# Kernel tuning notes

Hardware: AMD Instinct MI355X
Metric: run time of the kernel (lower is better)

Reference implementation:

```python
import jax, jax.numpy as jnp
import numpy as np

N = 100_000          # num nodes
E = 1_600_000        # undirected edges (mean_degree = 2E/N = 32)
Q = 8                # num_groups
NUM_ITER = 5         # fixed BP iterations (max_num_iter)


def setup_inputs() -> dict:
    key = jax.random.key(0)
    k1, k2, k3, k4 = jax.random.split(key, 4)
    u = jax.random.randint(k1, (E,), 0, N, dtype=jnp.int32)
    v = jax.random.randint(k2, (E,), 0, N, dtype=jnp.int32)
    # directed messages: both orientations of every undirected edge
    src = jnp.concatenate([u, v])                 # [2E] message source i of i->j
    dst = jnp.concatenate([v, u])                 # [2E] message target j of i->j
    # rev[e] = index of the reverse message j->i for edge e = i->j
    rev = jnp.concatenate([jnp.arange(E, 2 * E, dtype=jnp.int32),
                           jnp.arange(E, dtype=jnp.int32)])
    psi0 = jax.random.uniform(k3, (N, Q), dtype=jnp.float32)
    msg0 = jax.random.uniform(k4, (2 * E, Q), dtype=jnp.float32)
    c = 2.0 * E / N  # mean degree
    beta = jnp.asarray(np.log(Q / np.sqrt(c - 1.0) + 1.0), dtype=jnp.float32)
    return dict(beta=beta, psi0=psi0, msg0=msg0, src=src, dst=dst, rev=rev,
                num_iter=NUM_ITER)


def reference(beta, psi0, msg0, src, dst, rev, num_iter):
    N_, Q_ = psi0.shape
    M = msg0.shape[0]
    mean_w = M / (N_ * N_)  # adjacency_matrix.mean() = 2E / N^2 (unweighted)
    psi = psi0 / psi0.sum(1, keepdims=True)   # normalized marginals [N,Q]
    msg = msg0 / msg0.sum(1, keepdims=True)   # normalized messages  [M,Q]
    h = (-beta * mean_w * psi).sum(0)         # external field        [Q]

    def step(carry, _):
        msg, psi, h = carry
        c = jnp.expm1(beta)                          # e^beta - 1
        # per-incoming-edge factor, in log space (scatter_mul -> segment_sum of logs)
        log_f = jnp.log1p(msg * c)                   # [M,Q]
        S = jax.ops.segment_sum(log_f, dst, num_segments=N_)  # [N,Q] prod over k->i
        # message i->j: exclude contribution of reverse edge j->i (cavity)
        logits = h + S[src] - log_f[rev]             # [M,Q]
        new_msg = jax.nn.softmax(logits, axis=-1)    # normalized per message
        diff = jnp.max(jnp.abs(new_msg - msg))
        # marginals from updated messages
        log_f2 = jnp.log1p(new_msg * c)
        S2 = jax.ops.segment_sum(log_f2, dst, num_segments=N_)
        new_psi = jax.nn.softmax(h + S2, axis=-1)    # [N,Q]
        new_h = (-beta * mean_w * new_psi).sum(0)    # [Q]
        return (new_msg, new_psi, new_h), diff

    (msg, psi, h), diffs = jax.lax.scan(step, (msg, psi, h), None, length=int(num_iter))
    return msg, psi, diffs[-1]
```

## Files before the change

### kernel.cpp

```cpp
#include <hip/hip_runtime.h>
#include <math.h>

#define Q 8
#define NUM_ITER 5
#define BLOCK 256
#define EBLK 1024
#define BLOCKA 512
#define NBN 1024
#define NBSHIFT 10
#define MAXBKT 128
#define W 4
#define QS 262144.0f
#define GRED 512

__device__ __forceinline__ void load8(const float* __restrict__ p, float v[Q]) {
    float4 a = ((const float4*)p)[0];
    float4 b = ((const float4*)p)[1];
    v[0]=a.x; v[1]=a.y; v[2]=a.z; v[3]=a.w;
    v[4]=b.x; v[5]=b.y; v[6]=b.z; v[7]=b.w;
}

__device__ __forceinline__ void store8(float* __restrict__ p, const float v[Q]) {
    ((float4*)p)[0] = make_float4(v[0],v[1],v[2],v[3]);
    ((float4*)p)[1] = make_float4(v[4],v[5],v[6],v[7]);
}

__device__ __forceinline__ void softmax8_fast(float l[Q]) {
    float mx = l[0];
    #pragma unroll
    for (int q=1;q<Q;q++) mx = fmaxf(mx, l[q]);
    float s = 0.f;
    #pragma unroll
    for (int q=0;q<Q;q++) { l[q] = __expf(l[q]-mx); s += l[q]; }
    float inv = 1.0f/s;
    #pragma unroll
    for (int q=0;q<Q;q++) l[q] *= inv;
}

__device__ __forceinline__ void pack18(const float lf[Q], int loc, uint4& a, unsigned& x) {
    unsigned v[Q];
    #pragma unroll
    for (int q=0;q<Q;q++) v[q] = (unsigned)__float2int_rn(lf[q]*QS);
    a.x = (v[0]&0xFFFFu) | ((v[1]&0xFFFFu)<<16);
    a.y = (v[2]&0xFFFFu) | ((v[3]&0xFFFFu)<<16);
    a.z = (v[4]&0xFFFFu) | ((v[5]&0xFFFFu)<<16);
    a.w = (v[6]&0xFFFFu) | ((v[7]&0xFFFFu)<<16);
    x = (v[0]>>16) | ((v[1]>>16)<<2) | ((v[2]>>16)<<4) | ((v[3]>>16)<<6)
      | ((v[4]>>16)<<8) | ((v[5]>>16)<<10) | ((v[6]>>16)<<12) | ((v[7]>>16)<<14)
      | ((unsigned)loc<<16);
}

__device__ __forceinline__ void dq18(uint4 a, unsigned x, float lf[Q]) {
    lf[0] = (float)((a.x & 0xFFFFu) | ((x     &3u)<<16)) * (1.0f/QS);
    lf[1] = (float)((a.x >> 16)     | (((x>>2 )&3u)<<16)) * (1.0f/QS);
    lf[2] = (float)((a.y & 0xFFFFu) | (((x>>4 )&3u)<<16)) * (1.0f/QS);
    lf[3] = (float)((a.y >> 16)     | (((x>>6 )&3u)<<16)) * (1.0f/QS);
    lf[4] = (float)((a.z & 0xFFFFu) | (((x>>8 )&3u)<<16)) * (1.0f/QS);
    lf[5] = (float)((a.z >> 16)     | (((x>>10)&3u)<<16)) * (1.0f/QS);
    lf[6] = (float)((a.w & 0xFFFFu) | (((x>>12)&3u)<<16)) * (1.0f/QS);
    lf[7] = (float)((a.w >> 16)     | (((x>>14)&3u)<<16)) * (1.0f/QS);
}

__global__ __launch_bounds__(EBLK) void k_cnt2(const int* __restrict__ src,
                                               const int* __restrict__ dst,
                                               int* __restrict__ gcnt, int E) {
    __shared__ int cnt[MAXBKT];
    int tid = threadIdx.x;
    for (int t=tid; t<MAXBKT; t+=EBLK) cnt[t]=0;
    __syncthreads();
    int k = blockIdx.x*EBLK + tid;
    if (k < E) {
        atomicAdd(&cnt[dst[k]>>NBSHIFT], 1);
        atomicAdd(&cnt[src[k]>>NBSHIFT], 1);
    }
    __syncthreads();
    for (int t=tid; t<MAXBKT; t+=EBLK) gcnt[(size_t)blockIdx.x*MAXBKT + t] = cnt[t];
}

__global__ __launch_bounds__(256) void k_scan2(const int* __restrict__ gcnt,
                                               int* __restrict__ erel,
                                               int* __restrict__ btot, int nblk) {
    int b = blockIdx.x;
    int t = threadIdx.x;
    int chunk = (nblk + 255) / 256;
    int lo = t*chunk, hi = lo+chunk; if (hi > nblk) hi = nblk; if (lo > nblk) lo = nblk;
    int s = 0;
    for (int i=lo;i<hi;++i) s += gcnt[(size_t)i*MAXBKT + b];
    __shared__ int part[256];
    part[t] = s;
    __syncthreads();
    for (int off=1; off<256; off<<=1) {
        int v = (t>=off) ? part[t-off] : 0;
        __syncthreads();
        part[t] += v;
        __syncthreads();
    }
    int base = (t==0) ? 0 : part[t-1];
    for (int i=lo;i<hi;++i) {
        int c = gcnt[(size_t)i*MAXBKT + b];
        erel[(size_t)i*MAXBKT + b] = base;
        base += c;
    }
    if (t==255) btot[b] = part[255];
}

__global__ void k_scan(const int* __restrict__ btot, int* __restrict__ bucket_start,
                       int nbkt) {
    if (threadIdx.x==0 && blockIdx.x==0) {
        int run = 0;
        for (int b=0;b<nbkt;b++) { bucket_start[b]=run; run += btot[b]; }
        bucket_start[nbkt] = run;
    }
}

__global__ void k_psi_init(const float* __restrict__ psi0,
                           const float* __restrict__ beta_p,
                           float mean_w, double* __restrict__ h0, int N) {
    int i = blockIdx.x*BLOCK + threadIdx.x;
    float c[Q];
    #pragma unroll
    for (int q=0;q<Q;q++) c[q]=0.f;
    if (i < N) {
        float p[Q]; load8(psi0 + (size_t)i*Q, p);
        float s = 0.f;
        #pragma unroll
        for (int q=0;q<Q;q++) s += p[q];
        float scale = -beta_p[0]*mean_w/s;
        #pragma unroll
        for (int q=0;q<Q;q++) c[q] = p[q]*scale;
    }
    __shared__ double sm[BLOCK/64][Q];
    #pragma unroll
    for (int q=0;q<Q;q++) {
        double x = (double)c[q];
        #pragma unroll
        for (int off=32;off;off>>=1) x += __shfl_down(x,off);
        if ((threadIdx.x&63)==0) sm[threadIdx.x>>6][q]=x;
    }
    __syncthreads();
    if (threadIdx.x < Q) {
        double x = sm[0][threadIdx.x]+sm[1][threadIdx.x]+sm[2][threadIdx.x]+sm[3][threadIdx.x];
        atomicAdd(h0+threadIdx.x, x);
    }
}

__global__ __launch_bounds__(EBLK) void k_init(const float* __restrict__ msg0,
                       const int* __restrict__ src, const int* __restrict__ dst,
                       const float* __restrict__ beta_p,
                       uint4* __restrict__ lfe_q, unsigned* __restrict__ lfe_x,
                       uint4* __restrict__ ebuf_q, unsigned* __restrict__ ebuf_x,
                       const int* __restrict__ erel,
                       const int* __restrict__ bucket_start_g, int E) {
    __shared__ int cnt[MAXBKT], excl[MAXBKT], base[MAXBKT];
    __shared__ int totsh;
    __shared__ uint4 staged[2*EBLK];
    __shared__ unsigned staged_x[2*EBLK];
    __shared__ int gpos[2*EBLK];
    int tid = threadIdx.x;
    for (int t=tid; t<MAXBKT; t+=EBLK) cnt[t]=0;
    if (tid < MAXBKT) base[tid] = bucket_start_g[tid] + erel[(size_t)blockIdx.x*MAXBKT + tid];
    __syncthreads();
    int k = blockIdx.x*EBLK + tid;
    bool act = (k < E);
    int b1=0,b2=0,o1=0,o2=0;
    uint4 p1, p2; unsigned x1, x2;
    if (act) {
        float cc = expm1f(beta_p[0]);
        int i = src[k], j = dst[k];
        float a[Q], b[Q];
        load8(msg0 + (size_t)k*Q, a);
        load8(msg0 + ((size_t)k+E)*Q, b);
        float sa=0.f, sb=0.f;
        #pragma unroll
        for (int q=0;q<Q;q++) { sa += a[q]; sb += b[q]; }
        float ia = 1.0f/sa, ib = 1.0f/sb;
        #pragma unroll
        for (int q=0;q<Q;q++) { a[q]*=ia; b[q]*=ib; }
        float lfa[Q], lfb[Q];
        #pragma unroll
        for (int q=0;q<Q;q++) {
            lfa[q] = __logf(fmaf(a[q], cc, 1.0f));
            lfb[q] = __logf(fmaf(b[q], cc, 1.0f));
        }
        b1 = j>>NBSHIFT; b2 = i>>NBSHIFT;
        o1 = atomicAdd(&cnt[b1], 1);
        o2 = atomicAdd(&cnt[b2], 1);
        pack18(lfa, j & (NBN-1), p1, x1);
        pack18(lfb, i & (NBN-1), p2, x2);
        lfe_q[k]   = p1; lfe_x[k]   = x1;
        lfe_q[k+E] = p2; lfe_x[k+E] = x2;
    }
    __syncthreads();
    if (tid < 64) {
        int a = cnt[2*tid], b = cnt[2*tid+1];
        int s = a+b;
        int incl = s;
        #pragma unroll
        for (int d=1; d<64; d<<=1) {
            int v = __shfl_up(incl, d);
            if (tid >= d) incl += v;
        }
        int exclp = incl - s;
        excl[2*tid]   = exclp;
        excl[2*tid+1] = exclp + a;
        if (tid==63) totsh = incl;
    }
    __syncthreads();
    if (act) {
        int s1 = excl[b1]+o1; staged[s1]=p1; staged_x[s1]=x1; gpos[s1]=base[b1]+o1;
        int s2 = excl[b2]+o2; staged[s2]=p2; staged_x[s2]=x2; gpos[s2]=base[b2]+o2;
    }
    __syncthreads();
    int total = totsh;
    for (int s=tid; s<total; s+=EBLK) {
        int g = gpos[s];
        ebuf_q[g] = staged[s];
        ebuf_x[g] = staged_x[s];
    }
}

template<bool LAST>
__global__ __launch_bounds__(EBLK) void k_edge(const int* __restrict__ src,
                       const int* __restrict__ dst,
                       const float* __restrict__ beta_p,
                       const double* __restrict__ h, const float* __restrict__ Sf,
                       uint4* __restrict__ lfe_q, unsigned* __restrict__ lfe_x,
                       float* __restrict__ out_msg,
                       uint4* __restrict__ ebuf_q, unsigned* __restrict__ ebuf_x,
                       const int* __restrict__ erel,
                       const int* __restrict__ bucket_start_g,
                       float* __restrict__ diff_out, int E) {
    __shared__ int cnt[MAXBKT], excl[MAXBKT], base[MAXBKT];
    __shared__ int totsh;
    __shared__ uint4 staged[2*EBLK];
    __shared__ unsigned staged_x[2*EBLK];
    __shared__ int gpos[2*EBLK];
    int tid = threadIdx.x;
    for (int t=tid; t<MAXBKT; t+=EBLK) cnt[t]=0;
    if (tid < MAXBKT) base[tid] = bucket_start_g[tid] + erel[(size_t)blockIdx.x*MAXBKT + tid];
    __syncthreads();
    int k = blockIdx.x*EBLK + tid;
    bool act = (k < E);
    float lmax = 0.f;
    int b1=0,b2=0,o1=0,o2=0;
    uint4 p1, p2; unsigned x1, x2;
    if (act) {
        float cc = expm1f(beta_p[0]);
        int i = src[k], j = dst[k];
        float lf1o[Q], lf2o[Q];
        dq18(lfe_q[k],   lfe_x[k],   lf1o);
        dq18(lfe_q[k+E], lfe_x[k+E], lf2o);
        float hv[Q];
        #pragma unroll
        for (int q=0;q<Q;q++) hv[q] = (float)h[q];
        float Si[Q], Sj[Q];
        load8(Sf + (size_t)i*Q, Si);
        load8(Sf + (size_t)j*Q, Sj);
        float l1[Q], l2[Q];
        #pragma unroll
        for (int q=0;q<Q;q++) {
            l1[q] = hv[q] + Si[q] - lf2o[q];
            l2[q] = hv[q] + Sj[q] - lf1o[q];
        }
        softmax8_fast(l1);
        softmax8_fast(l2);
        if (LAST) {
            float icc = 1.0f/cc;
            #pragma unroll
            for (int q=0;q<Q;q++) {
                float m1o = (__expf(lf1o[q]) - 1.0f) * icc;
                float m2o = (__expf(lf2o[q]) - 1.0f) * icc;
                lmax = fmaxf(lmax, fabsf(l1[q]-m1o));
                lmax = fmaxf(lmax, fabsf(l2[q]-m2o));
            }
            store8(out_msg + (size_t)k*Q,     l1);
            store8(out_msg + ((size_t)k+E)*Q, l2);
        }
        float lf1n[Q], lf2n[Q];
        #pragma unroll
        for (int q=0;q<Q;q++) {
            lf1n[q] = __logf(fmaf(l1[q], cc, 1.0f));
            lf2n[q] = __logf(fmaf(l2[q], cc, 1.0f));
        }
        b1 = j>>NBSHIFT; b2 = i>>NBSHIFT;
        o1 = atomicAdd(&cnt[b1], 1);
        o2 = atomicAdd(&cnt[b2], 1);
        pack18(lf1n, j & (NBN-1), p1, x1);
        pack18(lf2n, i & (NBN-1), p2, x2);
        lfe_q[k]   = p1; lfe_x[k]   = x1;
        lfe_q[k+E] = p2; lfe_x[k+E] = x2;
    }
    __syncthreads();
    if (tid < 64) {
        int a = cnt[2*tid], b = cnt[2*tid+1];
        int s = a+b;
        int incl = s;
        #pragma unroll
        for (int d=1; d<64; d<<=1) {
            int v = __shfl_up(incl, d);
            if (tid >= d) incl += v;
        }
        int exclp = incl - s;
        excl[2*tid]   = exclp;
        excl[2*tid+1] = exclp + a;
        if (tid==63) totsh = incl;
    }
    __syncthreads();
    if (act) {
        int s1 = excl[b1]+o1; staged[s1]=p1; staged_x[s1]=x1; gpos[s1]=base[b1]+o1;
        int s2 = excl[b2]+o2; staged[s2]=p2; staged_x[s2]=x2; gpos[s2]=base[b2]+o2;
    }
    __syncthreads();
    int total = totsh;
    for (int s=tid; s<total; s+=EBLK) {
        int g = gpos[s];
        ebuf_q[g] = staged[s];
        ebuf_x[g] = staged_x[s];
    }
    if (LAST) {
        float x = lmax;
        #pragma unroll
        for (int off=32;off;off>>=1) x = fmaxf(x, __shfl_down(x,off));
        __shared__ float smx[EBLK/64];
        if ((tid&63)==0) smx[tid>>6]=x;
        __syncthreads();
        if (tid==0) {
            float bmax = smx[0];
            #pragma unroll
            for (int t=1;t<EBLK/64;t++) bmax = fmaxf(bmax, smx[t]);
            atomicMax((unsigned int*)diff_out, __float_as_uint(bmax));
        }
    }
}

__global__ __launch_bounds__(BLOCKA) void k_accum(const uint4* __restrict__ ebuf_q,
                                                  const unsigned* __restrict__ ebuf_x,
                                                  const int* __restrict__ bucket_start,
                                                  unsigned long long* __restrict__ partials) {
    __shared__ unsigned long long Sl[NBN*4];
    int wg = blockIdx.x;
    int b = wg / W, w = wg % W;
    for (int t=threadIdx.x*4; t<NBN*8; t+=BLOCKA*4) *(int4*)((int*)Sl+t) = make_int4(0,0,0,0);
    __syncthreads();
    int lo = bucket_start[b], hi = bucket_start[b+1];
    int len = hi - lo;
    int l0 = lo + (int)(((long long)len * w) / W);
    int l1 = lo + (int)(((long long)len * (w+1)) / W);
    for (int s = l0 + threadIdx.x; s < l1; s += BLOCKA) {
        uint4 v = ebuf_q[s];
        unsigned x = ebuf_x[s];
        int loc = (int)(x >> 16);
        unsigned long long v0 = (v.x&0xFFFFu) | ((x&3u)<<16);
        unsigned long long v1 = (v.x>>16)     | (((x>>2)&3u)<<16);
        unsigned long long v2 = (v.y&0xFFFFu) | (((x>>4)&3u)<<16);
        unsigned long long v3 = (v.y>>16)     | (((x>>6)&3u)<<16);
        unsigned long long v4 = (v.z&0xFFFFu) | (((x>>8)&3u)<<16);
        unsigned long long v5 = (v.z>>16)     | (((x>>10)&3u)<<16);
        unsigned long long v6 = (v.w&0xFFFFu) | (((x>>12)&3u)<<16);
        unsigned long long v7 = (v.w>>16)     | (((x>>14)&3u)<<16);
        unsigned long long* p = Sl + loc*4;
        atomicAdd(p+0, v0 | (v1<<32));
        atomicAdd(p+1, v2 | (v3<<32));
        atomicAdd(p+2, v4 | (v5<<32));
        atomicAdd(p+3, v6 | (v7<<32));
    }
    __syncthreads();
    unsigned long long* outp = partials + (size_t)wg * (NBN*4);
    for (int t=threadIdx.x*4; t<NBN*8; t+=BLOCKA*4) *(int4*)((int*)outp+t) = *(const int4*)((const int*)Sl+t);
}

template<bool INIT, bool LAST>
__global__ __launch_bounds__(BLOCK) void k_reduce(const unsigned* __restrict__ pu,
                         const double* __restrict__ hcur,
                         const float* __restrict__ beta_p,
                         float mean_w, double* __restrict__ hnext,
                         float* __restrict__ Sf, float* __restrict__ psi_out, int N) {
    int q = threadIdx.x & 7;
    float hq = 0.f;
    if (!INIT) hq = (float)hcur[q];
    double pacc = 0.0;
    int total = N*8;
    int stride = BLOCK*GRED;
    for (int gid = blockIdx.x*BLOCK + threadIdx.x; gid < total; gid += stride) {
        int i = gid >> 3;
        int b = i >> NBSHIFT, loc = i & (NBN-1);
        unsigned s = 0;
        #pragma unroll
        for (int w=0; w<W; ++w) s += pu[(size_t)(b*W+w)*(NBN*8) + loc*8 + q];
        float Sv = (float)s * (1.0f/QS);
        Sf[gid] = Sv;
        if (!INIT) {
            float l = hq + Sv;
            float mx = l;
            #pragma unroll
            for (int m8=1;m8<8;m8<<=1) mx = fmaxf(mx, __shfl_xor(mx, m8));
            float ex = __expf(l - mx);
            float sum = ex;
            #pragma unroll
            for (int m8=1;m8<8;m8<<=1) sum += __shfl_xor(sum, m8);
            float p = ex / sum;
            if (LAST) psi_out[gid] = p;
            pacc += (double)p;
        }
    }
    if (!INIT) {
        double x = pacc;
        #pragma unroll
        for (int m8=8;m8<64;m8<<=1) x += __shfl_xor(x, m8);
        __shared__ double sm[BLOCK/64][Q];
        if ((threadIdx.x&63) < Q) sm[threadIdx.x>>6][threadIdx.x&7] = x;
        __syncthreads();
        if (threadIdx.x < Q) {
            double t = sm[0][threadIdx.x]+sm[1][threadIdx.x]+sm[2][threadIdx.x]+sm[3][threadIdx.x];
            double scale = -(double)beta_p[0]*(double)mean_w;
            atomicAdd(hnext+threadIdx.x, t*scale);
        }
    }
}

extern "C" void kernel_launch(void* const* d_in, const int* in_sizes, int n_in,
                              void* d_out, int out_size, void* d_ws, size_t ws_size,
                              hipStream_t stream) {
    const float* beta = (const float*)d_in[0];
    const float* psi0 = (const float*)d_in[1];
    const float* msg0 = (const float*)d_in[2];
    const int*   src  = (const int*)d_in[3];
    const int*   dst  = (const int*)d_in[4];

    int N = in_sizes[1] / Q;
    int M = in_sizes[2] / Q;
    int E = M / 2;
    int nbkt = (N + NBN - 1) / NBN;
    float mean_w = (float)((double)M / ((double)N * (double)N));

    float* out_msg  = (float*)d_out;
    float* out_psi  = out_msg + (size_t)M*Q;
    float* out_diff = out_psi + (size_t)N*Q;

    int geE = (E + EBLK-1)/EBLK;

    char* p = (char*)d_ws;
    double* hb[2];
    hb[0] = (double*)p;                      p += 2*Q*sizeof(double);
    hb[1] = hb[0] + Q;
    unsigned long long* partials = (unsigned long long*)p;  p += (size_t)nbkt*W*NBN*4*sizeof(unsigned long long);
    float* Sf = (float*)p;                   p += (size_t)N*Q*sizeof(float);
    uint4* lfe_q = (uint4*)p;                p += (size_t)M*sizeof(uint4);
    uint4* ebuf_q = (uint4*)p;               p += (size_t)M*sizeof(uint4);
    unsigned* lfe_x = (unsigned*)p;          p += (size_t)M*sizeof(unsigned);
    unsigned* ebuf_x = (unsigned*)p;         p += (size_t)M*sizeof(unsigned);
    int* gcnt = (int*)p;                     p += (size_t)geE*MAXBKT*sizeof(int);
    int* erel = (int*)p;                     p += (size_t)geE*MAXBKT*sizeof(int);
    int* btot = (int*)p;                     p += MAXBKT*sizeof(int);
    int* bucket_start = (int*)p;             p += (MAXBKT+1)*sizeof(int);

    int gn   = (N + BLOCK-1)/BLOCK;
    int gacc = nbkt * W;

    hipMemsetAsync(hb[0], 0, Q*sizeof(double), stream);

    k_cnt2<<<geE,EBLK,0,stream>>>(src, dst, gcnt, E);
    k_scan2<<<nbkt,256,0,stream>>>(gcnt, erel, btot, geE);
    k_scan<<<1,64,0,stream>>>(btot, bucket_start, nbkt);

    k_init<<<geE,EBLK,0,stream>>>(msg0, src, dst, beta, lfe_q, lfe_x, ebuf_q, ebuf_x,
                                  erel, bucket_start, E);
    k_psi_init<<<gn,BLOCK,0,stream>>>(psi0, beta, mean_w, hb[0], N);
    k_accum<<<gacc,BLOCKA,0,stream>>>(ebuf_q, ebuf_x, bucket_start, partials);
    k_reduce<true,false><<<GRED,BLOCK,0,stream>>>((const unsigned*)partials, hb[0], beta,
                                                  mean_w, hb[1], Sf, out_psi, N);

    int cur = 0;
    for (int t=0; t<NUM_ITER; ++t) {
        int nxt = cur^1;
        hipMemsetAsync(hb[nxt], 0, Q*sizeof(double), stream);
        if (t == NUM_ITER-1) {
            hipMemsetAsync(out_diff, 0, sizeof(float), stream);
            k_edge<true ><<<geE,EBLK,0,stream>>>(src,dst,beta,hb[cur],Sf,lfe_q,lfe_x,out_msg,
                                                 ebuf_q,ebuf_x,erel,bucket_start,out_diff,E);
            k_accum<<<gacc,BLOCKA,0,stream>>>(ebuf_q, ebuf_x, bucket_start, partials);
            k_reduce<false,true ><<<GRED,BLOCK,0,stream>>>((const unsigned*)partials, hb[cur], beta,
                                                           mean_w, hb[nxt], Sf, out_psi, N);
        } else {
            k_edge<false><<<geE,EBLK,0,stream>>>(src,dst,beta,hb[cur],Sf,lfe_q,lfe_x,out_msg,
                                                 ebuf_q,ebuf_x,erel,bucket_start,out_diff,E);
            k_accum<<<gacc,BLOCKA,0,stream>>>(ebuf_q, ebuf_x, bucket_start, partials);
            k_reduce<false,false><<<GRED,BLOCK,0,stream>>>((const unsigned*)partials, hb[cur], beta,
                                                           mean_w, hb[nxt], Sf, out_psi, N);
        }
        cur = nxt;
    }
}
```

Baseline: 579.3 us.

## Cache bucketed scatter positions once in init and reuse them in edge kernels

The init kernel now computes each edge's destination slot in the bucketed edge buffer with shared atomics, writes straight to global memory, and records both slots in a new per-edge position array. The iterative edge kernel loads these cached positions and scatters directly. This drops the per-iteration shared-memory counting, block scan, staging and three barriers. In exchange the scatter writes are no longer grouped by bucket within the block, so they are less coalesced, and each edge reads an extra 8 bytes per iteration.

```diff
diff --git a/kernel.cpp b/kernel.cpp
--- a/kernel.cpp
+++ b/kernel.cpp
@@ -149,22 +149,18 @@
                        const float* __restrict__ beta_p,
                        uint4* __restrict__ lfe_q, unsigned* __restrict__ lfe_x,
                        uint4* __restrict__ ebuf_q, unsigned* __restrict__ ebuf_x,
+                       int2* __restrict__ epos,
                        const int* __restrict__ erel,
                        const int* __restrict__ bucket_start_g, int E) {
-    __shared__ int cnt[MAXBKT], excl[MAXBKT], base[MAXBKT];
-    __shared__ int totsh;
-    __shared__ uint4 staged[2*EBLK];
-    __shared__ unsigned staged_x[2*EBLK];
-    __shared__ int gpos[2*EBLK];
+    __shared__ int cnt[MAXBKT], base[MAXBKT];
     int tid = threadIdx.x;
-    for (int t=tid; t<MAXBKT; t+=EBLK) cnt[t]=0;
-    if (tid < MAXBKT) base[tid] = bucket_start_g[tid] + erel[(size_t)blockIdx.x*MAXBKT + tid];
+    if (tid < MAXBKT) {
+        cnt[tid] = 0;
+        base[tid] = bucket_start_g[tid] + erel[(size_t)blockIdx.x*MAXBKT + tid];
+    }
     __syncthreads();
     int k = blockIdx.x*EBLK + tid;
-    bool act = (k < E);
-    int b1=0,b2=0,o1=0,o2=0;
-    uint4 p1, p2; unsigned x1, x2;
-    if (act) {
+    if (k < E) {
         float cc = expm1f(beta_p[0]);
         int i = src[k], j = dst[k];
         float a[Q], b[Q];
@@ -182,40 +178,17 @@
             lfa[q] = __logf(fmaf(a[q], cc, 1.0f));
             lfb[q] = __logf(fmaf(b[q], cc, 1.0f));
         }
-        b1 = j>>NBSHIFT; b2 = i>>NBSHIFT;
-        o1 = atomicAdd(&cnt[b1], 1);
-        o2 = atomicAdd(&cnt[b2], 1);
+        uint4 p1, p2; unsigned x1, x2;
         pack18(lfa, j & (NBN-1), p1, x1);
         pack18(lfb, i & (NBN-1), p2, x2);
         lfe_q[k]   = p1; lfe_x[k]   = x1;
         lfe_q[k+E] = p2; lfe_x[k+E] = x2;
-    }
-    __syncthreads();
-    if (tid < 64) {
-        int a = cnt[2*tid], b = cnt[2*tid+1];
-        int s = a+b;
-        int incl = s;
-        #pragma unroll
-        for (int d=1; d<64; d<<=1) {
-            int v = __shfl_up(incl, d);
-            if (tid >= d) incl += v;
-        }
-        int exclp = incl - s;
-        excl[2*tid]   = exclp;
-        excl[2*tid+1] = exclp + a;
-        if (tid==63) totsh = incl;
-    }
-    __syncthreads();
-    if (act) {
-        int s1 = excl[b1]+o1; staged[s1]=p1; staged_x[s1]=x1; gpos[s1]=base[b1]+o1;
-        int s2 = excl[b2]+o2; staged[s2]=p2; staged_x[s2]=x2; gpos[s2]=base[b2]+o2;
-    }
-    __syncthreads();
-    int total = totsh;
-    for (int s=tid; s<total; s+=EBLK) {
-        int g = gpos[s];
-        ebuf_q[g] = staged[s];
-        ebuf_x[g] = staged_x[s];
+        int b1 = j>>NBSHIFT, b2 = i>>NBSHIFT;
+        int g1 = base[b1] + atomicAdd(&cnt[b1], 1);
+        int g2 = base[b2] + atomicAdd(&cnt[b2], 1);
+        ebuf_q[g1] = p1; ebuf_x[g1] = x1;
+        ebuf_q[g2] = p2; ebuf_x[g2] = x2;
+        epos[k] = make_int2(g1, g2);
     }
 }
 
@@ -227,24 +200,12 @@
                        uint4* __restrict__ lfe_q, unsigned* __restrict__ lfe_x,
                        float* __restrict__ out_msg,
                        uint4* __restrict__ ebuf_q, unsigned* __restrict__ ebuf_x,
-                       const int* __restrict__ erel,
-                       const int* __restrict__ bucket_start_g,
+                       const int2* __restrict__ epos,
                        float* __restrict__ diff_out, int E) {
-    __shared__ int cnt[MAXBKT], excl[MAXBKT], base[MAXBKT];
-    __shared__ int totsh;
-    __shared__ uint4 staged[2*EBLK];
-    __shared__ unsigned staged_x[2*EBLK];
-    __shared__ int gpos[2*EBLK];
     int tid = threadIdx.x;
-    for (int t=tid; t<MAXBKT; t+=EBLK) cnt[t]=0;
-    if (tid < MAXBKT) base[tid] = bucket_start_g[tid] + erel[(size_t)blockIdx.x*MAXBKT + tid];
-    __syncthreads();
     int k = blockIdx.x*EBLK + tid;
-    bool act = (k < E);
     float lmax = 0.f;
-    int b1=0,b2=0,o1=0,o2=0;
-    uint4 p1, p2; unsigned x1, x2;
-    if (act) {
+    if (k < E) {
         float cc = expm1f(beta_p[0]);
         int i = src[k], j = dst[k];
         float lf1o[Q], lf2o[Q];
@@ -282,40 +243,14 @@
             lf1n[q] = __logf(fmaf(l1[q], cc, 1.0f));
             lf2n[q] = __logf(fmaf(l2[q], cc, 1.0f));
         }
-        b1 = j>>NBSHIFT; b2 = i>>NBSHIFT;
-        o1 = atomicAdd(&cnt[b1], 1);
-        o2 = atomicAdd(&cnt[b2], 1);
+        uint4 p1, p2; unsigned x1, x2;
         pack18(lf1n, j & (NBN-1), p1, x1);
         pack18(lf2n, i & (NBN-1), p2, x2);
         lfe_q[k]   = p1; lfe_x[k]   = x1;
         lfe_q[k+E] = p2; lfe_x[k+E] = x2;
-    }
-    __syncthreads();
-    if (tid < 64) {
-        int a = cnt[2*tid], b = cnt[2*tid+1];
-        int s = a+b;
-        int incl = s;
-        #pragma unroll
-        for (int d=1; d<64; d<<=1) {
-            int v = __shfl_up(incl, d);
-            if (tid >= d) incl += v;
-        }
-        int exclp = incl - s;
-        excl[2*tid]   = exclp;
-        excl[2*tid+1] = exclp + a;
-        if (tid==63) totsh = incl;
-    }
-    __syncthreads();
-    if (act) {
-        int s1 = excl[b1]+o1; staged[s1]=p1; staged_x[s1]=x1; gpos[s1]=base[b1]+o1;
-        int s2 = excl[b2]+o2; staged[s2]=p2; staged_x[s2]=x2; gpos[s2]=base[b2]+o2;
-    }
-    __syncthreads();
-    int total = totsh;
-    for (int s=tid; s<total; s+=EBLK) {
-        int g = gpos[s];
-        ebuf_q[g] = staged[s];
-        ebuf_x[g] = staged_x[s];
+        int2 gp = epos[k];
+        ebuf_q[gp.x] = p1; ebuf_x[gp.x] = x1;
+        ebuf_q[gp.y] = p2; ebuf_x[gp.y] = x2;
     }
     if (LAST) {
         float x = lmax;
@@ -449,6 +384,7 @@
     uint4* ebuf_q = (uint4*)p;               p += (size_t)M*sizeof(uint4);
     unsigned* lfe_x = (unsigned*)p;          p += (size_t)M*sizeof(unsigned);
     unsigned* ebuf_x = (unsigned*)p;         p += (size_t)M*sizeof(unsigned);
+    int2* epos = (int2*)p;                   p += (size_t)E*sizeof(int2);
     int* gcnt = (int*)p;                     p += (size_t)geE*MAXBKT*sizeof(int);
     int* erel = (int*)p;                     p += (size_t)geE*MAXBKT*sizeof(int);
     int* btot = (int*)p;                     p += MAXBKT*sizeof(int);
@@ -464,7 +400,7 @@
     k_scan<<<1,64,0,stream>>>(btot, bucket_start, nbkt);
 
     k_init<<<geE,EBLK,0,stream>>>(msg0, src, dst, beta, lfe_q, lfe_x, ebuf_q, ebuf_x,
-                                  erel, bucket_start, E);
+                                  epos, erel, bucket_start, E);
     k_psi_init<<<gn,BLOCK,0,stream>>>(psi0, beta, mean_w, hb[0], N);
     k_accum<<<gacc,BLOCKA,0,stream>>>(ebuf_q, ebuf_x, bucket_start, partials);
     k_reduce<true,false><<<GRED,BLOCK,0,stream>>>((const unsigned*)partials, hb[0], beta,
@@ -477,13 +413,13 @@
         if (t == NUM_ITER-1) {
             hipMemsetAsync(out_diff, 0, sizeof(float), stream);
             k_edge<true ><<<geE,EBLK,0,stream>>>(src,dst,beta,hb[cur],Sf,lfe_q,lfe_x,out_msg,
-                                                 ebuf_q,ebuf_x,erel,bucket_start,out_diff,E);
+                                                 ebuf_q,ebuf_x,epos,out_diff,E);
             k_accum<<<gacc,BLOCKA,0,stream>>>(ebuf_q, ebuf_x, bucket_start, partials);
             k_reduce<false,true ><<<GRED,BLOCK,0,stream>>>((const unsigned*)partials, hb[cur], beta,
                                                            mean_w, hb[nxt], Sf, out_psi, N);
         } else {
             k_edge<false><<<geE,EBLK,0,stream>>>(src,dst,beta,hb[cur],Sf,lfe_q,lfe_x,out_msg,
-                                                 ebuf_q,ebuf_x,erel,bucket_start,out_diff,E);
+                                                 ebuf_q,ebuf_x,epos,out_diff,E);
             k_accum<<<gacc,BLOCKA,0,stream>>>(ebuf_q, ebuf_x, bucket_start, partials);
             k_reduce<false,false><<<GRED,BLOCK,0,stream>>>((const unsigned*)partials, hb[cur], beta,
                                                            mean_w, hb[nxt], Sf, out_psi, N);
```

Result: slower. 700.4 us (+20.9%).

## Map one directed message per thread in edge kernel, exchanging reverse via lane shuffle

Applied to the files above, without the earlier changes.

The edge kernel now gives each thread one directed message instead of both orientations of an undirected edge. Lanes 0-31 handle the forward direction and lanes 32-63 the reverse direction of the same pair, and the reverse log-factor and node are exchanged with a cross-half-wave shuffle. The per-block pair count drops to 512 so that the bucket counts from the preprocessing kernels still match the edge kernel's block partition. This doubles thread count and lowers per-thread register and shared-memory use to raise occupancy and parallelism, at the cost of more blocks and finer-grained scatter staging.

```diff
diff --git a/kernel.cpp b/kernel.cpp
--- a/kernel.cpp
+++ b/kernel.cpp
@@ -4,7 +4,8 @@
 #define Q 8
 #define NUM_ITER 5
 #define BLOCK 256
-#define EBLK 1024
+#define PBLK 512
+#define EBLKT 1024
 #define BLOCKA 512
 #define NBN 1024
 #define NBSHIFT 10
@@ -61,20 +62,20 @@
     lf[7] = (float)((a.w >> 16)     | (((x>>14)&3u)<<16)) * (1.0f/QS);
 }
 
-__global__ __launch_bounds__(EBLK) void k_cnt2(const int* __restrict__ src,
+__global__ __launch_bounds__(PBLK) void k_cnt2(const int* __restrict__ src,
                                                const int* __restrict__ dst,
                                                int* __restrict__ gcnt, int E) {
     __shared__ int cnt[MAXBKT];
     int tid = threadIdx.x;
-    for (int t=tid; t<MAXBKT; t+=EBLK) cnt[t]=0;
-    __syncthreads();
-    int k = blockIdx.x*EBLK + tid;
-    if (k < E) {
-        atomicAdd(&cnt[dst[k]>>NBSHIFT], 1);
-        atomicAdd(&cnt[src[k]>>NBSHIFT], 1);
-    }
-    __syncthreads();
-    for (int t=tid; t<MAXBKT; t+=EBLK) gcnt[(size_t)blockIdx.x*MAXBKT + t] = cnt[t];
+    if (tid < MAXBKT) cnt[tid]=0;
+    __syncthreads();
+    int p = blockIdx.x*PBLK + tid;
+    if (p < E) {
+        atomicAdd(&cnt[dst[p]>>NBSHIFT], 1);
+        atomicAdd(&cnt[src[p]>>NBSHIFT], 1);
+    }
+    __syncthreads();
+    if (tid < MAXBKT) gcnt[(size_t)blockIdx.x*MAXBKT + tid] = cnt[tid];
 }
 
 __global__ __launch_bounds__(256) void k_scan2(const int* __restrict__ gcnt,
@@ -144,7 +145,7 @@
     }
 }
 
-__global__ __launch_bounds__(EBLK) void k_init(const float* __restrict__ msg0,
+__global__ __launch_bounds__(PBLK) void k_init(const float* __restrict__ msg0,
                        const int* __restrict__ src, const int* __restrict__ dst,
                        const float* __restrict__ beta_p,
                        uint4* __restrict__ lfe_q, unsigned* __restrict__ lfe_x,
@@ -153,23 +154,25 @@
                        const int* __restrict__ bucket_start_g, int E) {
     __shared__ int cnt[MAXBKT], excl[MAXBKT], base[MAXBKT];
     __shared__ int totsh;
-    __shared__ uint4 staged[2*EBLK];
-    __shared__ unsigned staged_x[2*EBLK];
-    __shared__ int gpos[2*EBLK];
+    __shared__ uint4 staged[2*PBLK];
+    __shared__ unsigned staged_x[2*PBLK];
+    __shared__ int gpos[2*PBLK];
     int tid = threadIdx.x;
-    for (int t=tid; t<MAXBKT; t+=EBLK) cnt[t]=0;
-    if (tid < MAXBKT) base[tid] = bucket_start_g[tid] + erel[(size_t)blockIdx.x*MAXBKT + tid];
-    __syncthreads();
-    int k = blockIdx.x*EBLK + tid;
-    bool act = (k < E);
+    if (tid < MAXBKT) {
+        cnt[tid] = 0;
+        base[tid] = bucket_start_g[tid] + erel[(size_t)blockIdx.x*MAXBKT + tid];
+    }
+    __syncthreads();
+    int p = blockIdx.x*PBLK + tid;
+    bool act = (p < E);
     int b1=0,b2=0,o1=0,o2=0;
     uint4 p1, p2; unsigned x1, x2;
     if (act) {
         float cc = expm1f(beta_p[0]);
-        int i = src[k], j = dst[k];
+        int i = src[p], j = dst[p];
         float a[Q], b[Q];
-        load8(msg0 + (size_t)k*Q, a);
-        load8(msg0 + ((size_t)k+E)*Q, b);
+        load8(msg0 + (size_t)p*Q, a);
+        load8(msg0 + ((size_t)p+E)*Q, b);
         float sa=0.f, sb=0.f;
         #pragma unroll
         for (int q=0;q<Q;q++) { sa += a[q]; sb += b[q]; }
@@ -182,13 +185,13 @@
             lfa[q] = __logf(fmaf(a[q], cc, 1.0f));
             lfb[q] = __logf(fmaf(b[q], cc, 1.0f));
         }
+        pack18(lfa, j & (NBN-1), p1, x1);
+        pack18(lfb, i & (NBN-1), p2, x2);
+        lfe_q[p]   = p1; lfe_x[p]   = x1;
+        lfe_q[p+E] = p2; lfe_x[p+E] = x2;
         b1 = j>>NBSHIFT; b2 = i>>NBSHIFT;
         o1 = atomicAdd(&cnt[b1], 1);
         o2 = atomicAdd(&cnt[b2], 1);
-        pack18(lfa, j & (NBN-1), p1, x1);
-        pack18(lfb, i & (NBN-1), p2, x2);
-        lfe_q[k]   = p1; lfe_x[k]   = x1;
-        lfe_q[k+E] = p2; lfe_x[k+E] = x2;
     }
     __syncthreads();
     if (tid < 64) {
@@ -212,7 +215,7 @@
     }
     __syncthreads();
     int total = totsh;
-    for (int s=tid; s<total; s+=EBLK) {
+    for (int s=tid; s<total; s+=PBLK) {
         int g = gpos[s];
         ebuf_q[g] = staged[s];
         ebuf_x[g] = staged_x[s];
@@ -220,8 +223,7 @@
 }
 
 template<bool LAST>
-__global__ __launch_bounds__(EBLK) void k_edge(const int* __restrict__ src,
-                       const int* __restrict__ dst,
+__global__ __launch_bounds__(EBLKT) void k_edge(const int* __restrict__ src,
                        const float* __restrict__ beta_p,
                        const double* __restrict__ h, const float* __restrict__ Sf,
                        uint4* __restrict__ lfe_q, unsigned* __restrict__ lfe_x,
@@ -232,63 +234,57 @@
                        float* __restrict__ diff_out, int E) {
     __shared__ int cnt[MAXBKT], excl[MAXBKT], base[MAXBKT];
     __shared__ int totsh;
-    __shared__ uint4 staged[2*EBLK];
-    __shared__ unsigned staged_x[2*EBLK];
-    __shared__ int gpos[2*EBLK];
+    __shared__ uint4 staged[EBLKT];
+    __shared__ unsigned staged_x[EBLKT];
+    __shared__ int gpos[EBLKT];
     int tid = threadIdx.x;
-    for (int t=tid; t<MAXBKT; t+=EBLK) cnt[t]=0;
-    if (tid < MAXBKT) base[tid] = bucket_start_g[tid] + erel[(size_t)blockIdx.x*MAXBKT + tid];
-    __syncthreads();
-    int k = blockIdx.x*EBLK + tid;
-    bool act = (k < E);
+    if (tid < MAXBKT) {
+        cnt[tid] = 0;
+        base[tid] = bucket_start_g[tid] + erel[(size_t)blockIdx.x*MAXBKT + tid];
+    }
+    __syncthreads();
+    int wave = tid >> 6;
+    int lane = tid & 63;
+    int d    = lane >> 5;
+    int pp   = blockIdx.x*PBLK + wave*32 + (lane & 31);
+    bool act = (pp < E);
     float lmax = 0.f;
-    int b1=0,b2=0,o1=0,o2=0;
-    uint4 p1, p2; unsigned x1, x2;
+    int bkt=0, off=0;
+    uint4 pk; unsigned xk;
     if (act) {
         float cc = expm1f(beta_p[0]);
-        int i = src[k], j = dst[k];
-        float lf1o[Q], lf2o[Q];
-        dq18(lfe_q[k],   lfe_x[k],   lf1o);
-        dq18(lfe_q[k+E], lfe_x[k+E], lf2o);
+        int idx = pp + d*E;
+        int node = src[idx];
+        float lfo[Q];
+        dq18(lfe_q[idx], lfe_x[idx], lfo);
+        float lfr[Q];
+        #pragma unroll
+        for (int q=0;q<Q;q++) lfr[q] = __shfl_xor(lfo[q], 32);
+        int node_other = __shfl_xor(node, 32);
         float hv[Q];
         #pragma unroll
         for (int q=0;q<Q;q++) hv[q] = (float)h[q];
-        float Si[Q], Sj[Q];
-        load8(Sf + (size_t)i*Q, Si);
-        load8(Sf + (size_t)j*Q, Sj);
-        float l1[Q], l2[Q];
-        #pragma unroll
-        for (int q=0;q<Q;q++) {
-            l1[q] = hv[q] + Si[q] - lf2o[q];
-            l2[q] = hv[q] + Sj[q] - lf1o[q];
-        }
-        softmax8_fast(l1);
-        softmax8_fast(l2);
+        float Sv[Q]; load8(Sf + (size_t)node*Q, Sv);
+        float l[Q];
+        #pragma unroll
+        for (int q=0;q<Q;q++) l[q] = hv[q] + Sv[q] - lfr[q];
+        softmax8_fast(l);
         if (LAST) {
             float icc = 1.0f/cc;
             #pragma unroll
             for (int q=0;q<Q;q++) {
-                float m1o = (__expf(lf1o[q]) - 1.0f) * icc;
-                float m2o = (__expf(lf2o[q]) - 1.0f) * icc;
-                lmax = fmaxf(lmax, fabsf(l1[q]-m1o));
-                lmax = fmaxf(lmax, fabsf(l2[q]-m2o));
+                float mo = (__expf(lfo[q]) - 1.0f) * icc;
+                lmax = fmaxf(lmax, fabsf(l[q]-mo));
             }
-            store8(out_msg + (size_t)k*Q,     l1);
-            store8(out_msg + ((size_t)k+E)*Q, l2);
-        }
-        float lf1n[Q], lf2n[Q];
-        #pragma unroll
-        for (int q=0;q<Q;q++) {
-            lf1n[q] = __logf(fmaf(l1[q], cc, 1.0f));
-            lf2n[q] = __logf(fmaf(l2[q], cc, 1.0f));
-        }
-        b1 = j>>NBSHIFT; b2 = i>>NBSHIFT;
-        o1 = atomicAdd(&cnt[b1], 1);
-        o2 = atomicAdd(&cnt[b2], 1);
-        pack18(lf1n, j & (NBN-1), p1, x1);
-        pack18(lf2n, i & (NBN-1), p2, x2);
-        lfe_q[k]   = p1; lfe_x[k]   = x1;
-        lfe_q[k+E] = p2; lfe_x[k+E] = x2;
+            store8(out_msg + (size_t)idx*Q, l);
+        }
+        float lfn[Q];
+        #pragma unroll
+        for (int q=0;q<Q;q++) lfn[q] = __logf(fmaf(l[q], cc, 1.0f));
+        pack18(lfn, node_other & (NBN-1), pk, xk);
+        lfe_q[idx] = pk; lfe_x[idx] = xk;
+        bkt = node_other >> NBSHIFT;
+        off = atomicAdd(&cnt[bkt], 1);
     }
     __syncthreads();
     if (tid < 64) {
@@ -296,9 +292,9 @@
         int s = a+b;
         int incl = s;
         #pragma unroll
-        for (int d=1; d<64; d<<=1) {
-            int v = __shfl_up(incl, d);
-            if (tid >= d) incl += v;
+        for (int dd=1; dd<64; dd<<=1) {
+            int v = __shfl_up(incl, dd);
+            if (tid >= dd) incl += v;
         }
         int exclp = incl - s;
         excl[2*tid]   = exclp;
@@ -307,12 +303,12 @@
     }
     __syncthreads();
     if (act) {
-        int s1 = excl[b1]+o1; staged[s1]=p1; staged_x[s1]=x1; gpos[s1]=base[b1]+o1;
-        int s2 = excl[b2]+o2; staged[s2]=p2; staged_x[s2]=x2; gpos[s2]=base[b2]+o2;
+        int s1 = excl[bkt]+off;
+        staged[s1]=pk; staged_x[s1]=xk; gpos[s1]=base[bkt]+off;
     }
     __syncthreads();
     int total = totsh;
-    for (int s=tid; s<total; s+=EBLK) {
+    for (int s=tid; s<total; s+=EBLKT) {
         int g = gpos[s];
         ebuf_q[g] = staged[s];
         ebuf_x[g] = staged_x[s];
@@ -320,14 +316,14 @@
     if (LAST) {
         float x = lmax;
         #pragma unroll
-        for (int off=32;off;off>>=1) x = fmaxf(x, __shfl_down(x,off));
-        __shared__ float smx[EBLK/64];
+        for (int o2=32;o2;o2>>=1) x = fmaxf(x, __shfl_down(x,o2));
+        __shared__ float smx[EBLKT/64];
         if ((tid&63)==0) smx[tid>>6]=x;
         __syncthreads();
         if (tid==0) {
             float bmax = smx[0];
             #pragma unroll
-            for (int t=1;t<EBLK/64;t++) bmax = fmaxf(bmax, smx[t]);
+            for (int t=1;t<EBLKT/64;t++) bmax = fmaxf(bmax, smx[t]);
             atomicMax((unsigned int*)diff_out, __float_as_uint(bmax));
         }
     }
@@ -437,7 +433,7 @@
     float* out_psi  = out_msg + (size_t)M*Q;
     float* out_diff = out_psi + (size_t)N*Q;
 
-    int geE = (E + EBLK-1)/EBLK;
+    int geP = (E + PBLK-1)/PBLK;
 
     char* p = (char*)d_ws;
     double* hb[2];
@@ -449,8 +445,8 @@
     uint4* ebuf_q = (uint4*)p;               p += (size_t)M*sizeof(uint4);
     unsigned* lfe_x = (unsigned*)p;          p += (size_t)M*sizeof(unsigned);
     unsigned* ebuf_x = (unsigned*)p;         p += (size_t)M*sizeof(unsigned);
-    int* gcnt = (int*)p;                     p += (size_t)geE*MAXBKT*sizeof(int);
-    int* erel = (int*)p;                     p += (size_t)geE*MAXBKT*sizeof(int);
+    int* gcnt = (int*)p;                     p += (size_t)geP*MAXBKT*sizeof(int);
+    int* erel = (int*)p;                     p += (size_t)geP*MAXBKT*sizeof(int);
     int* btot = (int*)p;                     p += MAXBKT*sizeof(int);
     int* bucket_start = (int*)p;             p += (MAXBKT+1)*sizeof(int);
 
@@ -459,11 +455,11 @@
 
     hipMemsetAsync(hb[0], 0, Q*sizeof(double), stream);
 
-    k_cnt2<<<geE,EBLK,0,stream>>>(src, dst, gcnt, E);
-    k_scan2<<<nbkt,256,0,stream>>>(gcnt, erel, btot, geE);
+    k_cnt2<<<geP,PBLK,0,stream>>>(src, dst, gcnt, E);
+    k_scan2<<<nbkt,256,0,stream>>>(gcnt, erel, btot, geP);
     k_scan<<<1,64,0,stream>>>(btot, bucket_start, nbkt);
 
-    k_init<<<geE,EBLK,0,stream>>>(msg0, src, dst, beta, lfe_q, lfe_x, ebuf_q, ebuf_x,
+    k_init<<<geP,PBLK,0,stream>>>(msg0, src, dst, beta, lfe_q, lfe_x, ebuf_q, ebuf_x,
                                   erel, bucket_start, E);
     k_psi_init<<<gn,BLOCK,0,stream>>>(psi0, beta, mean_w, hb[0], N);
     k_accum<<<gacc,BLOCKA,0,stream>>>(ebuf_q, ebuf_x, bucket_start, partials);
@@ -476,14 +472,14 @@
         hipMemsetAsync(hb[nxt], 0, Q*sizeof(double), stream);
         if (t == NUM_ITER-1) {
             hipMemsetAsync(out_diff, 0, sizeof(float), stream);
-            k_edge<true ><<<geE,EBLK,0,stream>>>(src,dst,beta,hb[cur],Sf,lfe_q,lfe_x,out_msg,
-                                                 ebuf_q,ebuf_x,erel,bucket_start,out_diff,E);
+            k_edge<true ><<<geP,EBLKT,0,stream>>>(src,beta,hb[cur],Sf,lfe_q,lfe_x,out_msg,
+                                                  ebuf_q,ebuf_x,erel,bucket_start,out_diff,E);
             k_accum<<<gacc,BLOCKA,0,stream>>>(ebuf_q, ebuf_x, bucket_start, partials);
             k_reduce<false,true ><<<GRED,BLOCK,0,stream>>>((const unsigned*)partials, hb[cur], beta,
                                                            mean_w, hb[nxt], Sf, out_psi, N);
         } else {
-            k_edge<false><<<geE,EBLK,0,stream>>>(src,dst,beta,hb[cur],Sf,lfe_q,lfe_x,out_msg,
-                                                 ebuf_q,ebuf_x,erel,bucket_start,out_diff,E);
+            k_edge<false><<<geP,EBLKT,0,stream>>>(src,beta,hb[cur],Sf,lfe_q,lfe_x,out_msg,
+                                                  ebuf_q,ebuf_x,erel,bucket_start,out_diff,E);
             k_accum<<<gacc,BLOCKA,0,stream>>>(ebuf_q, ebuf_x, bucket_start, partials);
             k_reduce<false,false><<<GRED,BLOCK,0,stream>>>((const unsigned*)partials, hb[cur], beta,
                                                            mean_w, hb[nxt], Sf, out_psi, N);
```

After: 591.2 us. 1.02x slower.
